# Kernel optimization log

Measured on AMD Instinct MI355X. Metric: run time of the kernel, lower is better.

Reference implementation:

```python
import jax, jax.numpy as jnp
import numpy as np
from jax import lax

B, C, KH, SH, K = 128, 256, 7, 31, 3
EPS = 1e-5
DN = ('NCHW', 'OIHW', 'NCHW')


def _bn(x, p):
    # p: (4, C) rows = gamma, beta, running_mean, running_var (eval-mode BN)
    g, b, m, v = p[0], p[1], p[2], p[3]
    inv = g / jnp.sqrt(v + EPS)
    return x * inv[None, :, None, None] + (b - m * inv)[None, :, None, None]


def _dwconv(x, w):
    # depthwise 3x3 VALID conv, w: (C,1,K,K)
    return lax.conv_general_dilated(x, w, (1, 1), 'VALID', dimension_numbers=DN,
                                    feature_group_count=x.shape[1])


def _pwconv(x, w, b):
    y = lax.conv_general_dilated(x, w, (1, 1), 'VALID', dimension_numbers=DN)
    return y + b[None, :, None, None]


def _relu6(x):
    return jnp.minimum(jax.nn.relu(x), 6.0)


def _branch(x, dw_w, bn1, pw_w, pw_b, bn2):
    # Conv(dw,3x3,no bias) -> BN -> ReLU6 -> Conv(1x1) -> BN
    return _bn(_pwconv(_relu6(_bn(_dwconv(x, dw_w), bn1)), pw_w, pw_b), bn2)


def _xcorr_depthwise(search, kernel):
    # per-sample, per-channel cross-correlation via groups = B*C conv trick
    b, c, hs, ws = search.shape
    hk, wk = kernel.shape[2], kernel.shape[3]
    x = search.reshape(1, b * c, hs, ws)
    k = kernel.reshape(b * c, 1, hk, wk)
    out = lax.conv_general_dilated(x, k, (1, 1), 'VALID', dimension_numbers=DN,
                                   feature_group_count=b * c)
    return out.reshape(b, c, out.shape[2], out.shape[3])


def _bn_params(key):
    k1, k2, k3, k4 = jax.random.split(key, 4)
    g = jax.random.uniform(k1, (C,), minval=0.5, maxval=1.5)
    b = jax.random.normal(k2, (C,)) * 0.1
    m = jax.random.normal(k3, (C,)) * 0.1
    v = jax.random.uniform(k4, (C,), minval=0.5, maxval=1.5)
    return jnp.stack([g, b, m, v]).astype(jnp.float32)


def setup_inputs() -> dict:
    key = jax.random.key(0)
    ks = jax.random.split(key, 10)
    dw_std = np.float32(np.sqrt(2.0 / (K * K * C)))   # torch init: normal(0, sqrt(2/n))
    pw_std = np.float32(np.sqrt(2.0 / C))
    return {
        'kernel': jax.random.normal(ks[0], (B, C, KH, KH), jnp.float32),
        'search': jax.random.normal(ks[1], (B, C, SH, SH), jnp.float32),
        'k_dw_w': jax.random.normal(ks[2], (C, 1, K, K), jnp.float32) * dw_std,
        'k_bn1': _bn_params(ks[3]),
        'k_pw_w': jax.random.normal(ks[4], (C, C, 1, 1), jnp.float32) * pw_std,
        'k_pw_b': jnp.zeros((C,), jnp.float32),
        'k_bn2': _bn_params(ks[5]),
        's_dw_w': jax.random.normal(ks[6], (C, 1, K, K), jnp.float32) * dw_std,
        's_bn1': _bn_params(ks[7]),
        's_pw_w': jax.random.normal(ks[8], (C, C, 1, 1), jnp.float32) * pw_std,
        's_pw_b': jnp.zeros((C,), jnp.float32),
        's_bn2': _bn_params(ks[9]),
    }


def reference(kernel, search, k_dw_w, k_bn1, k_pw_w, k_pw_b, k_bn2,
              s_dw_w, s_bn1, s_pw_w, s_pw_b, s_bn2):
    k = _branch(kernel, k_dw_w, k_bn1, k_pw_w, k_pw_b, k_bn2)   # (B,C,5,5)
    s = _branch(search, s_dw_w, s_bn1, s_pw_w, s_pw_b, s_bn2)   # (B,C,29,29)
    return _xcorr_depthwise(s, k)                                # (B,C,25,25)
```

## Files before the change

### kernel.cpp

```cpp
#include <hip/hip_runtime.h>

constexpr int B = 128, C = 256;
constexpr float EPS = 1e-5f;
constexpr int NSG = B * 841;
constexpr int NKG = B * 25;

typedef unsigned short u16;
typedef short short8 __attribute__((ext_vector_type(8)));
typedef u16 u16x8 __attribute__((ext_vector_type(8)));
typedef float f32x4 __attribute__((ext_vector_type(4)));

__device__ __forceinline__ u16 bf16_rne(float x) {
    unsigned u = __builtin_bit_cast(unsigned, x);
    return (u16)((u + 0x7FFFu + ((u >> 16) & 1u)) >> 16);
}
__device__ __forceinline__ float bf16_f(u16 h) {
    return __builtin_bit_cast(float, (unsigned)h << 16);
}

__global__ __launch_bounds__(256)
void wprep3(const float* __restrict__ ws, const float* __restrict__ wk,
            u16* __restrict__ WtS, u16* __restrict__ WtK) {
    int i = blockIdx.x * 256 + threadIdx.x;
    int co = i >> 8, k = i & 255;
    int t = k >> 5, cg = co >> 4;
    int lane = ((k >> 3) & 3) * 16 + (co & 15);
    int e = k & 7;
    size_t o = ((size_t)(t * 16 + cg) * 64 + lane) * 8 + e;
    WtS[o] = bf16_rne(ws[i]);
    WtK[o] = bf16_rne(wk[i]);
}

template<int IN_H, int CG>
__global__ __launch_bounds__(256)
void dw_pass7(const float* __restrict__ in, const float* __restrict__ dw_w,
              const float* __restrict__ bn1, u16* __restrict__ X3) {
    constexpr int OUT_H = IN_H - 2, ON = OUT_H * OUT_H, IHW = IN_H * IN_H;
    constexpr int NSTRIP = (OUT_H + 7) / 8;
    constexpr int NFLT = CG * IHW;
    constexpr int NF4 = NFLT / 4;
    constexpr int SUBS = CG / 8;
    constexpr int NSP = B * ON;
    constexpr int PADC = CG + 2;
    constexpr unsigned SM_IN = (NFLT + 16) * 4;
    constexpr unsigned SM_XT = (unsigned)ON * PADC * 2;
    constexpr unsigned SMSZ = SM_IN > SM_XT ? SM_IN : SM_XT;
    __shared__ __align__(16) char SMEM[SMSZ];
    float* S = (float*)SMEM;
    u16* xt = (u16*)SMEM;

    const int tid = threadIdx.x;
    const int b = blockIdx.x, g = blockIdx.y;
    const int ci0 = g * CG;
    const float* src = in + ((size_t)b * C + ci0) * IHW;

    for (int q = tid; q < NF4; q += 256)
        ((float4*)S)[q] = ((const float4*)src)[q];
    __syncthreads();

    const bool active = tid < CG * OUT_H;
    int cl = 0, oh = 0;
    if (active) { cl = tid / OUT_H; oh = tid - cl * OUT_H; }
    u16 outv[NSTRIP][8];
    if (active) {
        const int ci = ci0 + cl;
        float wreg[9];
        #pragma unroll
        for (int q = 0; q < 9; ++q) wreg[q] = dw_w[ci * 9 + q];
        const float inv = bn1[ci] * rsqrtf(bn1[3 * C + ci] + EPS);
        const float shv = bn1[C + ci] - bn1[2 * C + ci] * inv;
        #pragma unroll
        for (int s = 0; s < NSTRIP; ++s) {
            float res[8] = {0.f, 0.f, 0.f, 0.f, 0.f, 0.f, 0.f, 0.f};
            #pragma unroll
            for (int dy = 0; dy < 3; ++dy) {
                const float* r = S + cl * IHW + (oh + dy) * IN_H + s * 8;
                float x[10];
                #pragma unroll
                for (int j = 0; j < 10; ++j) x[j] = r[j];
                #pragma unroll
                for (int o = 0; o < 8; ++o)
                    res[o] = fmaf(x[o], wreg[dy * 3],
                              fmaf(x[o + 1], wreg[dy * 3 + 1],
                               fmaf(x[o + 2], wreg[dy * 3 + 2], res[o])));
            }
            #pragma unroll
            for (int o = 0; o < 8; ++o) {
                float y = res[o] * inv + shv;
                y = fminf(fmaxf(y, 0.f), 6.f);
                outv[s][o] = bf16_rne(y);
            }
        }
    }
    __syncthreads();

    if (active) {
        #pragma unroll
        for (int s = 0; s < NSTRIP; ++s) {
            const int ow0 = s * 8;
            #pragma unroll
            for (int o = 0; o < 8; ++o) {
                if (ow0 + o < OUT_H) {
                    int n = oh * OUT_H + ow0 + o;
                    xt[n * PADC + cl] = outv[s][o];
                }
            }
        }
    }
    __syncthreads();

    for (int q = tid; q < ON * SUBS; q += 256) {
        int sub = q / ON, n = q - sub * ON;
        const unsigned* w = (const unsigned*)xt + n * (PADC / 2) + sub * 4;
        uint4 v = {w[0], w[1], w[2], w[3]};
        u16* dst = X3 + ((size_t)(g * SUBS + sub) * NSP + (size_t)b * ON + n) * 8;
        *(uint4*)dst = v;
    }
}

template<int PQ>
__global__ __launch_bounds__(256)
void gemm6(const u16* __restrict__ X3, const u16* __restrict__ Wt,
           const float* __restrict__ pw_b, const float* __restrict__ bn2,
           u16* __restrict__ out) {
    constexpr int NSP = B * PQ;
    const int lane = threadIdx.x & 63, wave = threadIdx.x >> 6;
    const int lh = lane >> 4, ll = lane & 15;
    const int n0 = blockIdx.x * 64;

    f32x4 acc[4][4] = {};

    #pragma unroll 1
    for (int t = 0; t < 8; ++t) {
        short8 aw[4], bx[4];
        #pragma unroll
        for (int j = 0; j < 4; ++j) {
            size_t off = ((size_t)(t * 4 + lh) * NSP + n0 + j * 16 + ll) * 8;
            bx[j] = *(const short8*)(X3 + off);
        }
        #pragma unroll
        for (int i = 0; i < 4; ++i) {
            int cg = wave * 4 + i;
            size_t off = ((size_t)(t * 16 + cg) * 64 + lane) * 8;
            aw[i] = *(const short8*)(Wt + off);
        }
        #pragma unroll
        for (int i = 0; i < 4; ++i)
            #pragma unroll
            for (int j = 0; j < 4; ++j)
                acc[i][j] = __builtin_amdgcn_mfma_f32_16x16x32_bf16(aw[i], bx[j], acc[i][j], 0, 0, 0);
    }

    int bj[4], pj[4];
    #pragma unroll
    for (int j = 0; j < 4; ++j) {
        int nn = n0 + j * 16 + ll;
        bj[j] = nn / PQ; pj[j] = nn - bj[j] * PQ;
    }
    #pragma unroll
    for (int i = 0; i < 4; ++i) {
        #pragma unroll
        for (int r = 0; r < 4; ++r) {
            int co = wave * 64 + i * 16 + lh * 4 + r;
            float inv = bn2[co] * rsqrtf(bn2[3 * C + co] + EPS);
            float sh  = bn2[C + co] - bn2[2 * C + co] * inv + pw_b[co] * inv;
            #pragma unroll
            for (int j = 0; j < 4; ++j)
                out[((size_t)bj[j] * C + co) * PQ + pj[j]] = bf16_rne(acc[i][j][r] * inv + sh);
        }
    }
}

__global__ __launch_bounds__(256)
void xcorr3(const u16* __restrict__ s, const u16* __restrict__ k,
            float* __restrict__ out) {
    const int bc0 = blockIdx.x * 10;
    const int nbc = min(10, B * C - bc0);
    __shared__ float ss[10 * 841];
    __shared__ float ks[10 * 25];
    const int tid = threadIdx.x;
    for (int i = tid; i < nbc * 841; i += 256) ss[i] = bf16_f(s[(size_t)bc0 * 841 + i]);
    for (int i = tid; i < nbc * 25; i += 256) ks[i] = bf16_f(k[(size_t)bc0 * 25 + i]);
    __syncthreads();

    const int lb = tid / 25, lt = tid - lb * 25;
    if (lb >= nbc) return;
    const int ohg = lt / 5, owg = lt - ohg * 5;
    const float* sp = ss + lb * 841 + (ohg * 5) * 29 + owg * 5;
    float kk[25];
    #pragma unroll
    for (int q = 0; q < 25; ++q) kk[q] = ks[lb * 25 + q];

    float acc[5][5] = {};
    #pragma unroll
    for (int ir = 0; ir < 9; ++ir) {
        float row[9];
        #pragma unroll
        for (int j = 0; j < 9; ++j) row[j] = sp[ir * 29 + j];
        #pragma unroll
        for (int oi = 0; oi < 5; ++oi) {
            int ki = ir - oi;
            if (ki < 0 || ki > 4) continue;
            #pragma unroll
            for (int oj = 0; oj < 5; ++oj)
                #pragma unroll
                for (int kj = 0; kj < 5; ++kj)
                    acc[oi][oj] = fmaf(row[oj + kj], kk[ki * 5 + kj], acc[oi][oj]);
        }
    }
    float* op = out + (size_t)(bc0 + lb) * 625;
    #pragma unroll
    for (int oi = 0; oi < 5; ++oi)
        #pragma unroll
        for (int oj = 0; oj < 5; ++oj)
            op[(ohg * 5 + oi) * 25 + owg * 5 + oj] = acc[oi][oj];
}

template<int IN_H>
__global__ __launch_bounds__(256)
void branch_fallback(const float* __restrict__ in, const float* __restrict__ dw_w,
                     const float* __restrict__ bn1, const float* __restrict__ pw_w,
                     const float* __restrict__ pw_b, const float* __restrict__ bn2,
                     float* __restrict__ out) {
    constexpr int OUT_H = IN_H - 2;
    constexpr int P = OUT_H * OUT_H;
    const int n0  = blockIdx.x * 64;
    const int co0 = blockIdx.y * 64;
    const int tid = threadIdx.x;
    const int tx = tid & 15, ty = tid >> 4;
    __shared__ __align__(16) float Ws[16][64];
    __shared__ __align__(16) float Xs2[16][64];
    float acc[4][4] = {};
    for (int k0 = 0; k0 < C; k0 += 16) {
        #pragma unroll
        for (int e = 0; e < 4; e++) {
            int idx = e * 256 + tid;
            int m = idx & 63, kk = idx >> 6;
            Ws[kk][m] = pw_w[(co0 + m) * C + (k0 + kk)];
        }
        #pragma unroll
        for (int e = 0; e < 4; e++) {
            int idx = e * 256 + tid;
            int nn = idx & 63, kk = idx >> 6;
            int ci = k0 + kk;
            int n = n0 + nn;
            int b = n / P, p = n - b * P;
            int oh = p / OUT_H, ow = p - oh * OUT_H;
            const float* ip = in + (((size_t)b * C + ci) * IN_H + oh) * IN_H + ow;
            const float* wp = dw_w + ci * 9;
            float s = 0.f;
            #pragma unroll
            for (int dy = 0; dy < 3; dy++)
                #pragma unroll
                for (int dx = 0; dx < 3; dx++)
                    s = fmaf(ip[dy * IN_H + dx], wp[dy * 3 + dx], s);
            float inv = bn1[ci] * rsqrtf(bn1[3 * C + ci] + EPS);
            float y = s * inv + (bn1[C + ci] - bn1[2 * C + ci] * inv);
            Xs2[kk][nn] = fminf(fmaxf(y, 0.f), 6.f);
        }
        __syncthreads();
        #pragma unroll
        for (int kk = 0; kk < 16; kk++) {
            float4 av = *reinterpret_cast<const float4*>(&Ws[kk][ty * 4]);
            float4 bv = *reinterpret_cast<const float4*>(&Xs2[kk][tx * 4]);
            float a[4] = {av.x, av.y, av.z, av.w};
            float bb[4] = {bv.x, bv.y, bv.z, bv.w};
            #pragma unroll
            for (int i = 0; i < 4; i++)
                #pragma unroll
                for (int j = 0; j < 4; j++)
                    acc[i][j] = fmaf(a[i], bb[j], acc[i][j]);
        }
        __syncthreads();
    }
    #pragma unroll
    for (int i = 0; i < 4; i++) {
        int co = co0 + ty * 4 + i;
        float inv = bn2[co] * rsqrtf(bn2[3 * C + co] + EPS);
        float sh  = (bn2[C + co] - bn2[2 * C + co] * inv) + pw_b[co] * inv;
        int n = n0 + tx * 4;
        #pragma unroll
        for (int j = 0; j < 4; j++) {
            int nj = n + j;
            int bj2 = nj / P, pj2 = nj - bj2 * P;
            out[((size_t)bj2 * C + co) * P + pj2] = acc[i][j] * inv + sh;
        }
    }
}

__global__ __launch_bounds__(256)
void xcorr2f(const float* __restrict__ s, const float* __restrict__ k,
             float* __restrict__ out) {
    const int bc0 = blockIdx.x * 10;
    const int nbc = min(10, B * C - bc0);
    __shared__ float ss[10 * 841];
    __shared__ float ks[10 * 25];
    const int tid = threadIdx.x;
    for (int i = tid; i < nbc * 841; i += 256) ss[i] = s[(size_t)bc0 * 841 + i];
    for (int i = tid; i < nbc * 25; i += 256) ks[i] = k[(size_t)bc0 * 25 + i];
    __syncthreads();
    const int lb = tid / 25, lt = tid - lb * 25;
    if (lb >= nbc) return;
    const int ohg = lt / 5, owg = lt - ohg * 5;
    const float* sp = ss + lb * 841 + (ohg * 5) * 29 + owg * 5;
    float kk[25];
    #pragma unroll
    for (int q = 0; q < 25; ++q) kk[q] = ks[lb * 25 + q];
    float acc[5][5] = {};
    #pragma unroll
    for (int ir = 0; ir < 9; ++ir) {
        float row[9];
        #pragma unroll
        for (int j = 0; j < 9; ++j) row[j] = sp[ir * 29 + j];
        #pragma unroll
        for (int oi = 0; oi < 5; ++oi) {
            int ki = ir - oi;
            if (ki < 0 || ki > 4) continue;
            #pragma unroll
            for (int oj = 0; oj < 5; ++oj)
                #pragma unroll
                for (int kj = 0; kj < 5; ++kj)
                    acc[oi][oj] = fmaf(row[oj + kj], kk[ki * 5 + kj], acc[oi][oj]);
        }
    }
    float* op = out + (size_t)(bc0 + lb) * 625;
    #pragma unroll
    for (int oi = 0; oi < 5; ++oi)
        #pragma unroll
        for (int oj = 0; oj < 5; ++oj)
            op[(ohg * 5 + oi) * 25 + owg * 5 + oj] = acc[oi][oj];
}

extern "C" void kernel_launch(void* const* d_in, const int* in_sizes, int n_in,
                              void* d_out, int out_size, void* d_ws, size_t ws_size,
                              hipStream_t stream) {
    const float* kernel = (const float*)d_in[0];
    const float* search = (const float*)d_in[1];
    const float* k_dw_w = (const float*)d_in[2];
    const float* k_bn1  = (const float*)d_in[3];
    const float* k_pw_w = (const float*)d_in[4];
    const float* k_pw_b = (const float*)d_in[5];
    const float* k_bn2  = (const float*)d_in[6];
    const float* s_dw_w = (const float*)d_in[7];
    const float* s_bn1  = (const float*)d_in[8];
    const float* s_pw_w = (const float*)d_in[9];
    const float* s_pw_b = (const float*)d_in[10];
    const float* s_bn2  = (const float*)d_in[11];

    constexpr size_t SB_B  = (size_t)NSG * C * 2;
    constexpr size_t KB_B  = (size_t)NKG * C * 2;
    constexpr size_t X3S_B = (size_t)NSG * 256;
    constexpr size_t X3S_BB = (size_t)NSG * C * 2;
    constexpr size_t X3K_BB = (size_t)NKG * C * 2;
    constexpr size_t W_B    = (size_t)C * C * 2;
    constexpr size_t NEED   = SB_B + KB_B + X3S_BB + X3K_BB + 2 * W_B;

    if (ws_size >= NEED) {
        char* base = (char*)d_ws;
        u16* Sb   = (u16*)base;   base += SB_B;
        u16* Kb   = (u16*)base;   base += KB_B;
        u16* X3s  = (u16*)base;   base += X3S_BB;
        u16* X3k  = (u16*)base;   base += X3K_BB;
        u16* WtS  = (u16*)base;   base += W_B;
        u16* WtK  = (u16*)base;

        wprep3<<<dim3(256), dim3(256), 0, stream>>>(s_pw_w, k_pw_w, WtS, WtK);
        dw_pass7<31, 8><<<dim3(B, 32), dim3(256), 0, stream>>>(search, s_dw_w, s_bn1, X3s);
        dw_pass7<7, 32><<<dim3(B, 8), dim3(256), 0, stream>>>(kernel, k_dw_w, k_bn1, X3k);
        gemm6<841><<<dim3(NSG / 64), dim3(256), 0, stream>>>(X3s, WtS, s_pw_b, s_bn2, Sb);
        gemm6<25><<<dim3(NKG / 64), dim3(256), 0, stream>>>(X3k, WtK, k_pw_b, k_bn2, Kb);
        xcorr3<<<dim3((B * C + 9) / 10), dim3(256), 0, stream>>>(Sb, Kb, (float*)d_out);
    } else {
        float* s_buf = (float*)d_ws;
        float* k_buf = s_buf + (size_t)B * C * 29 * 29;
        branch_fallback<7><<<dim3(50, 4), dim3(256), 0, stream>>>(
            kernel, k_dw_w, k_bn1, k_pw_w, k_pw_b, k_bn2, k_buf);
        branch_fallback<31><<<dim3(1682, 4), dim3(256), 0, stream>>>(
            search, s_dw_w, s_bn1, s_pw_w, s_pw_b, s_bn2, s_buf);
        xcorr2f<<<dim3((B * C + 9) / 10), dim3(256), 0, stream>>>(s_buf, k_buf, (float*)d_out);
    }
}
```

Measured before the change: 148.3 us.

## Double-buffer depthwise input via LDS async loads and software-pipeline GEMM loads

Adds a new depthwise kernel in which each block handles four channel slices, prefetching the next slice into a second LDS buffer with global_load_lds while computing the current one, so global load latency overlaps the depthwise compute. The GEMM kernel is rewritten with register double-buffering: operands for the next k-step are loaded before the MFMAs on the current ones. Cost: the search depthwise grid has a quarter as many blocks and uses more LDS (two 31x31x8 float buffers plus the transpose tile), which lowers parallelism and occupancy. It also holds more live registers in the GEMM.

```diff
diff --git a/kernel.cpp b/kernel.cpp
--- a/kernel.cpp
+++ b/kernel.cpp
@@ -17,6 +17,11 @@
 __device__ __forceinline__ float bf16_f(u16 h) {
     return __builtin_bit_cast(float, (unsigned)h << 16);
 }
+
+#define GLOAD16(g, l)                                                              \
+    __builtin_amdgcn_global_load_lds(                                              \
+        (const __attribute__((address_space(1))) unsigned int*)(g),                \
+        (__attribute__((address_space(3))) unsigned int*)(l), 16, 0, 0)
 
 __global__ __launch_bounds__(256)
 void wprep3(const float* __restrict__ ws, const float* __restrict__ wk,
@@ -29,6 +34,106 @@
     size_t o = ((size_t)(t * 16 + cg) * 64 + lane) * 8 + e;
     WtS[o] = bf16_rne(ws[i]);
     WtK[o] = bf16_rne(wk[i]);
+}
+
+template<int IN_H, int CG, int NSLICE>
+__global__ __launch_bounds__(256)
+void dw_pass8(const float* __restrict__ in, const float* __restrict__ dw_w,
+              const float* __restrict__ bn1, u16* __restrict__ X3) {
+    constexpr int OUT_H = IN_H - 2, ON = OUT_H * OUT_H, IHW = IN_H * IN_H;
+    constexpr int NSTRIP = (OUT_H + 7) / 8;
+    constexpr int NF4 = CG * IHW / 4;
+    constexpr int SUBS = CG / 8;
+    constexpr int NSP = B * ON;
+    constexpr int PADC = CG + 2;
+    __shared__ __align__(16) float S[2][NF4 * 4 + 16];
+    __shared__ __align__(16) u16 xt[ON * PADC];
+
+    const int tid = threadIdx.x;
+    const int b = blockIdx.x;
+    const int g0 = blockIdx.y * NSLICE;
+
+    const bool active = tid < CG * OUT_H;
+    int cl = 0, oh = 0;
+    if (active) { cl = tid / OUT_H; oh = tid - cl * OUT_H; }
+
+    auto issue_stage = [&](int buf, int g) {
+        const float* src = in + ((size_t)b * C + g * CG) * IHW;
+        #pragma unroll
+        for (int ii = 0; ii < (NF4 + 255) / 256; ++ii) {
+            int q = ii * 256 + tid;
+            if (q < NF4) GLOAD16(src + q * 4, (char*)S[buf] + q * 16);
+        }
+    };
+
+    issue_stage(0, g0);
+    int cur = 0;
+
+    for (int it = 0; it < NSLICE; ++it) {
+        const int g = g0 + it;
+        const int ci0 = g * CG;
+        asm volatile("s_waitcnt vmcnt(0)" ::: "memory");
+        __syncthreads();
+
+        if (it + 1 < NSLICE) issue_stage(cur ^ 1, g0 + it + 1);
+
+        u16 outv[NSTRIP][8];
+        if (active) {
+            const int ci = ci0 + cl;
+            float wreg[9];
+            #pragma unroll
+            for (int q = 0; q < 9; ++q) wreg[q] = dw_w[ci * 9 + q];
+            const float inv = bn1[ci] * rsqrtf(bn1[3 * C + ci] + EPS);
+            const float shv = bn1[C + ci] - bn1[2 * C + ci] * inv;
+            #pragma unroll
+            for (int s = 0; s < NSTRIP; ++s) {
+                float res[8] = {0.f, 0.f, 0.f, 0.f, 0.f, 0.f, 0.f, 0.f};
+                #pragma unroll
+                for (int dy = 0; dy < 3; ++dy) {
+                    const float* r = S[cur] + cl * IHW + (oh + dy) * IN_H + s * 8;
+                    float x[10];
+                    #pragma unroll
+                    for (int j = 0; j < 10; ++j) x[j] = r[j];
+                    #pragma unroll
+                    for (int o = 0; o < 8; ++o)
+                        res[o] = fmaf(x[o], wreg[dy * 3],
+                                  fmaf(x[o + 1], wreg[dy * 3 + 1],
+                                   fmaf(x[o + 2], wreg[dy * 3 + 2], res[o])));
+                }
+                #pragma unroll
+                for (int o = 0; o < 8; ++o) {
+                    float y = res[o] * inv + shv;
+                    y = fminf(fmaxf(y, 0.f), 6.f);
+                    outv[s][o] = bf16_rne(y);
+                }
+            }
+        }
+        __syncthreads();
+
+        if (active) {
+            #pragma unroll
+            for (int s = 0; s < NSTRIP; ++s) {
+                const int ow0 = s * 8;
+                #pragma unroll
+                for (int o = 0; o < 8; ++o) {
+                    if (ow0 + o < OUT_H) {
+                        int n = oh * OUT_H + ow0 + o;
+                        xt[n * PADC + cl] = outv[s][o];
+                    }
+                }
+            }
+        }
+        __syncthreads();
+
+        for (int q = tid; q < ON * SUBS; q += 256) {
+            int sub = q / ON, n = q - sub * ON;
+            const unsigned* w = (const unsigned*)xt + n * (PADC / 2) + sub * 4;
+            uint4 v = {w[0], w[1], w[2], w[3]};
+            u16* dst = X3 + ((size_t)(g * SUBS + sub) * NSP + (size_t)b * ON + n) * 8;
+            *(uint4*)dst = v;
+        }
+        cur ^= 1;
+    }
 }
 
 template<int IN_H, int CG>
@@ -120,7 +225,7 @@
 
 template<int PQ>
 __global__ __launch_bounds__(256)
-void gemm6(const u16* __restrict__ X3, const u16* __restrict__ Wt,
+void gemm7(const u16* __restrict__ X3, const u16* __restrict__ Wt,
            const float* __restrict__ pw_b, const float* __restrict__ bn2,
            u16* __restrict__ out) {
     constexpr int NSP = B * PQ;
@@ -129,27 +234,45 @@
     const int n0 = blockIdx.x * 64;
 
     f32x4 acc[4][4] = {};
-
-    #pragma unroll 1
-    for (int t = 0; t < 8; ++t) {
-        short8 aw[4], bx[4];
-        #pragma unroll
-        for (int j = 0; j < 4; ++j) {
-            size_t off = ((size_t)(t * 4 + lh) * NSP + n0 + j * 16 + ll) * 8;
-            bx[j] = *(const short8*)(X3 + off);
-        }
-        #pragma unroll
-        for (int i = 0; i < 4; ++i) {
-            int cg = wave * 4 + i;
-            size_t off = ((size_t)(t * 16 + cg) * 64 + lane) * 8;
-            aw[i] = *(const short8*)(Wt + off);
-        }
-        #pragma unroll
-        for (int i = 0; i < 4; ++i)
-            #pragma unroll
-            for (int j = 0; j < 4; ++j)
-                acc[i][j] = __builtin_amdgcn_mfma_f32_16x16x32_bf16(aw[i], bx[j], acc[i][j], 0, 0, 0);
-    }
+    short8 bx0[4], aw0[4], bx1[4], aw1[4];
+
+#define LOADX(t, bx)                                                            \
+    {                                                                           \
+        _Pragma("unroll")                                                       \
+        for (int j = 0; j < 4; ++j) {                                           \
+            size_t off = ((size_t)((t) * 4 + lh) * NSP + n0 + j * 16 + ll) * 8; \
+            bx[j] = *(const short8*)(X3 + off);                                 \
+        }                                                                       \
+    }
+#define LOADW(t, aw)                                                            \
+    {                                                                           \
+        _Pragma("unroll")                                                       \
+        for (int i = 0; i < 4; ++i) {                                           \
+            size_t off = ((size_t)((t) * 16 + wave * 4 + i) * 64 + lane) * 8;   \
+            aw[i] = *(const short8*)(Wt + off);                                 \
+        }                                                                       \
+    }
+#define MM(aw, bx)                                                              \
+    {                                                                           \
+        _Pragma("unroll")                                                       \
+        for (int i = 0; i < 4; ++i) {                                           \
+            _Pragma("unroll")                                                   \
+            for (int j = 0; j < 4; ++j)                                         \
+                acc[i][j] = __builtin_amdgcn_mfma_f32_16x16x32_bf16(aw[i], bx[j], acc[i][j], 0, 0, 0); \
+        }                                                                       \
+    }
+
+    LOADX(0, bx0); LOADW(0, aw0);
+    #pragma unroll
+    for (int tt = 0; tt < 8; tt += 2) {
+        if (tt + 1 < 8) { LOADX(tt + 1, bx1); LOADW(tt + 1, aw1); }
+        MM(aw0, bx0);
+        if (tt + 2 < 8) { LOADX(tt + 2, bx0); LOADW(tt + 2, aw0); }
+        if (tt + 1 < 8) { MM(aw1, bx1); }
+    }
+#undef LOADX
+#undef LOADW
+#undef MM
 
     int bj[4], pj[4];
     #pragma unroll
@@ -349,26 +472,25 @@
 
     constexpr size_t SB_B  = (size_t)NSG * C * 2;
     constexpr size_t KB_B  = (size_t)NKG * C * 2;
-    constexpr size_t X3S_B = (size_t)NSG * 256;
-    constexpr size_t X3S_BB = (size_t)NSG * C * 2;
-    constexpr size_t X3K_BB = (size_t)NKG * C * 2;
-    constexpr size_t W_B    = (size_t)C * C * 2;
-    constexpr size_t NEED   = SB_B + KB_B + X3S_BB + X3K_BB + 2 * W_B;
+    constexpr size_t X3S_B = (size_t)NSG * C * 2;
+    constexpr size_t X3K_B = (size_t)NKG * C * 2;
+    constexpr size_t W_B   = (size_t)C * C * 2;
+    constexpr size_t NEED  = SB_B + KB_B + X3S_B + X3K_B + 2 * W_B;
 
     if (ws_size >= NEED) {
         char* base = (char*)d_ws;
         u16* Sb   = (u16*)base;   base += SB_B;
         u16* Kb   = (u16*)base;   base += KB_B;
-        u16* X3s  = (u16*)base;   base += X3S_BB;
-        u16* X3k  = (u16*)base;   base += X3K_BB;
+        u16* X3s  = (u16*)base;   base += X3S_B;
+        u16* X3k  = (u16*)base;   base += X3K_B;
         u16* WtS  = (u16*)base;   base += W_B;
         u16* WtK  = (u16*)base;
 
         wprep3<<<dim3(256), dim3(256), 0, stream>>>(s_pw_w, k_pw_w, WtS, WtK);
-        dw_pass7<31, 8><<<dim3(B, 32), dim3(256), 0, stream>>>(search, s_dw_w, s_bn1, X3s);
+        dw_pass8<31, 8, 4><<<dim3(B, 8), dim3(256), 0, stream>>>(search, s_dw_w, s_bn1, X3s);
         dw_pass7<7, 32><<<dim3(B, 8), dim3(256), 0, stream>>>(kernel, k_dw_w, k_bn1, X3k);
-        gemm6<841><<<dim3(NSG / 64), dim3(256), 0, stream>>>(X3s, WtS, s_pw_b, s_bn2, Sb);
-        gemm6<25><<<dim3(NKG / 64), dim3(256), 0, stream>>>(X3k, WtK, k_pw_b, k_bn2, Kb);
+        gemm7<841><<<dim3(NSG / 64), dim3(256), 0, stream>>>(X3s, WtS, s_pw_b, s_bn2, Sb);
+        gemm7<25><<<dim3(NKG / 64), dim3(256), 0, stream>>>(X3k, WtK, k_pw_b, k_bn2, Kb);
         xcorr3<<<dim3((B * C + 9) / 10), dim3(256), 0, stream>>>(Sb, Kb, (float*)d_out);
     } else {
         float* s_buf = (float*)d_ws;
```

Result: faster. 142.6 us, median of 2 (-3.9%).

## Split search depthwise pass into row bands and double-buffer GEMM operand loads

Applied to the files above, without the earlier changes.

Adds a new search-branch depthwise kernel in which each thread computes one output column for one channel over an 8-row band. It streams input rows straight from global memory through a rolling 3-row register window instead of staging the whole tile in shared memory. The grid gains a band dimension, which gives more, smaller blocks. The pointwise GEMM now prefetches the next K-slice of operands into a second register set while the MFMAs on the current set run, so load latency can overlap compute at the cost of more registers.

```diff
diff --git a/kernel.cpp b/kernel.cpp
--- a/kernel.cpp
+++ b/kernel.cpp
@@ -29,6 +29,61 @@
     size_t o = ((size_t)(t * 16 + cg) * 64 + lane) * 8 + e;
     WtS[o] = bf16_rne(ws[i]);
     WtK[o] = bf16_rne(wk[i]);
+}
+
+template<int IN_H>
+__global__ __launch_bounds__(256)
+void dw_pass10(const float* __restrict__ in, const float* __restrict__ dw_w,
+               const float* __restrict__ bn1, u16* __restrict__ X3) {
+    constexpr int OUT_H = IN_H - 2, ON = OUT_H * OUT_H;
+    constexpr int NSP = B * ON;
+    constexpr int BAND = 8;
+    constexpr int PADC = 10;
+    __shared__ __align__(16) u16 xt[BAND * OUT_H * PADC];
+
+    const int tid = threadIdx.x;
+    const int b = blockIdx.x, kc = blockIdx.y;
+    const int oh0 = blockIdx.z * BAND;
+    const int ov = min(BAND, OUT_H - oh0);
+
+    const bool active = tid < 8 * OUT_H;
+    if (active) {
+        const int ci = tid / OUT_H;
+        const int ow = tid - ci * OUT_H;
+        const int cig = kc * 8 + ci;
+        float w0 = dw_w[cig * 9 + 0], w1 = dw_w[cig * 9 + 1], w2 = dw_w[cig * 9 + 2];
+        float w3 = dw_w[cig * 9 + 3], w4 = dw_w[cig * 9 + 4], w5 = dw_w[cig * 9 + 5];
+        float w6 = dw_w[cig * 9 + 6], w7 = dw_w[cig * 9 + 7], w8 = dw_w[cig * 9 + 8];
+        const float inv = bn1[cig] * rsqrtf(bn1[3 * C + cig] + EPS);
+        const float shv = bn1[C + cig] - bn1[2 * C + cig] * inv;
+        const float* base = in + (((size_t)b * C + cig) * IN_H + oh0) * IN_H + ow;
+
+        float a0 = base[0],        a1 = base[1],        a2 = base[2];
+        float b0 = base[IN_H],     b1 = base[IN_H + 1], b2 = base[IN_H + 2];
+        #pragma unroll
+        for (int o = 0; o < BAND; ++o) {
+            if (o < ov) {
+                const float* rp = base + (o + 2) * IN_H;
+                float c0 = rp[0], c1 = rp[1], c2 = rp[2];
+                float res = a0 * w0 + a1 * w1 + a2 * w2
+                          + b0 * w3 + b1 * w4 + b2 * w5
+                          + c0 * w6 + c1 * w7 + c2 * w8;
+                float y = res * inv + shv;
+                y = fminf(fmaxf(y, 0.f), 6.f);
+                xt[(o * OUT_H + ow) * PADC + ci] = bf16_rne(y);
+                a0 = b0; a1 = b1; a2 = b2;
+                b0 = c0; b1 = c1; b2 = c2;
+            }
+        }
+    }
+    __syncthreads();
+
+    const int nv = ov * OUT_H;
+    for (int q = tid; q < nv; q += 256) {
+        const unsigned* wp = (const unsigned*)xt + q * (PADC / 2);
+        uint4 v = {wp[0], wp[1], wp[2], wp[3]};
+        *(uint4*)(X3 + ((size_t)kc * NSP + (size_t)b * ON + oh0 * OUT_H + q) * 8) = v;
+    }
 }
 
 template<int IN_H, int CG>
@@ -120,7 +175,7 @@
 
 template<int PQ>
 __global__ __launch_bounds__(256)
-void gemm6(const u16* __restrict__ X3, const u16* __restrict__ Wt,
+void gemm7(const u16* __restrict__ X3, const u16* __restrict__ Wt,
            const float* __restrict__ pw_b, const float* __restrict__ bn2,
            u16* __restrict__ out) {
     constexpr int NSP = B * PQ;
@@ -129,27 +184,45 @@
     const int n0 = blockIdx.x * 64;
 
     f32x4 acc[4][4] = {};
-
-    #pragma unroll 1
-    for (int t = 0; t < 8; ++t) {
-        short8 aw[4], bx[4];
-        #pragma unroll
-        for (int j = 0; j < 4; ++j) {
-            size_t off = ((size_t)(t * 4 + lh) * NSP + n0 + j * 16 + ll) * 8;
-            bx[j] = *(const short8*)(X3 + off);
-        }
-        #pragma unroll
-        for (int i = 0; i < 4; ++i) {
-            int cg = wave * 4 + i;
-            size_t off = ((size_t)(t * 16 + cg) * 64 + lane) * 8;
-            aw[i] = *(const short8*)(Wt + off);
-        }
-        #pragma unroll
-        for (int i = 0; i < 4; ++i)
-            #pragma unroll
-            for (int j = 0; j < 4; ++j)
-                acc[i][j] = __builtin_amdgcn_mfma_f32_16x16x32_bf16(aw[i], bx[j], acc[i][j], 0, 0, 0);
-    }
+    short8 bx0[4], aw0[4], bx1[4], aw1[4];
+
+#define LOADX(t, bx)                                                            \
+    {                                                                           \
+        _Pragma("unroll")                                                       \
+        for (int j = 0; j < 4; ++j) {                                           \
+            size_t off = ((size_t)((t) * 4 + lh) * NSP + n0 + j * 16 + ll) * 8; \
+            bx[j] = *(const short8*)(X3 + off);                                 \
+        }                                                                       \
+    }
+#define LOADW(t, aw)                                                            \
+    {                                                                           \
+        _Pragma("unroll")                                                       \
+        for (int i = 0; i < 4; ++i) {                                           \
+            size_t off = ((size_t)((t) * 16 + wave * 4 + i) * 64 + lane) * 8;   \
+            aw[i] = *(const short8*)(Wt + off);                                 \
+        }                                                                       \
+    }
+#define MM(aw, bx)                                                              \
+    {                                                                           \
+        _Pragma("unroll")                                                       \
+        for (int i = 0; i < 4; ++i) {                                           \
+            _Pragma("unroll")                                                   \
+            for (int j = 0; j < 4; ++j)                                         \
+                acc[i][j] = __builtin_amdgcn_mfma_f32_16x16x32_bf16(aw[i], bx[j], acc[i][j], 0, 0, 0); \
+        }                                                                       \
+    }
+
+    LOADX(0, bx0); LOADW(0, aw0);
+    #pragma unroll
+    for (int tt = 0; tt < 8; tt += 2) {
+        if (tt + 1 < 8) { LOADX(tt + 1, bx1); LOADW(tt + 1, aw1); }
+        MM(aw0, bx0);
+        if (tt + 2 < 8) { LOADX(tt + 2, bx0); LOADW(tt + 2, aw0); }
+        if (tt + 1 < 8) { MM(aw1, bx1); }
+    }
+#undef LOADX
+#undef LOADW
+#undef MM
 
     int bj[4], pj[4];
     #pragma unroll
@@ -349,26 +422,25 @@
 
     constexpr size_t SB_B  = (size_t)NSG * C * 2;
     constexpr size_t KB_B  = (size_t)NKG * C * 2;
-    constexpr size_t X3S_B = (size_t)NSG * 256;
-    constexpr size_t X3S_BB = (size_t)NSG * C * 2;
-    constexpr size_t X3K_BB = (size_t)NKG * C * 2;
-    constexpr size_t W_B    = (size_t)C * C * 2;
-    constexpr size_t NEED   = SB_B + KB_B + X3S_BB + X3K_BB + 2 * W_B;
+    constexpr size_t X3S_B = (size_t)NSG * C * 2;
+    constexpr size_t X3K_B = (size_t)NKG * C * 2;
+    constexpr size_t W_B   = (size_t)C * C * 2;
+    constexpr size_t NEED  = SB_B + KB_B + X3S_B + X3K_B + 2 * W_B;
 
     if (ws_size >= NEED) {
         char* base = (char*)d_ws;
         u16* Sb   = (u16*)base;   base += SB_B;
         u16* Kb   = (u16*)base;   base += KB_B;
-        u16* X3s  = (u16*)base;   base += X3S_BB;
-        u16* X3k  = (u16*)base;   base += X3K_BB;
+        u16* X3s  = (u16*)base;   base += X3S_B;
+        u16* X3k  = (u16*)base;   base += X3K_B;
         u16* WtS  = (u16*)base;   base += W_B;
         u16* WtK  = (u16*)base;
 
         wprep3<<<dim3(256), dim3(256), 0, stream>>>(s_pw_w, k_pw_w, WtS, WtK);
-        dw_pass7<31, 8><<<dim3(B, 32), dim3(256), 0, stream>>>(search, s_dw_w, s_bn1, X3s);
+        dw_pass10<31><<<dim3(B, 32, 4), dim3(256), 0, stream>>>(search, s_dw_w, s_bn1, X3s);
         dw_pass7<7, 32><<<dim3(B, 8), dim3(256), 0, stream>>>(kernel, k_dw_w, k_bn1, X3k);
-        gemm6<841><<<dim3(NSG / 64), dim3(256), 0, stream>>>(X3s, WtS, s_pw_b, s_bn2, Sb);
-        gemm6<25><<<dim3(NKG / 64), dim3(256), 0, stream>>>(X3k, WtK, k_pw_b, k_bn2, Kb);
+        gemm7<841><<<dim3(NSG / 64), dim3(256), 0, stream>>>(X3s, WtS, s_pw_b, s_bn2, Sb);
+        gemm7<25><<<dim3(NKG / 64), dim3(256), 0, stream>>>(X3k, WtK, k_pw_b, k_bn2, Kb);
         xcorr3<<<dim3((B * C + 9) / 10), dim3(256), 0, stream>>>(Sb, Kb, (float*)d_out);
     } else {
         float* s_buf = (float*)d_ws;
```

Measured after the change: 163.6 us. 10.3% more time.
